# Optimization experiments

Hardware: AMD Instinct MI355X
Metric: run time of the kernel (lower is better)

Reference implementation:

```python
import jax, jax.numpy as jnp
import numpy as np

N = 16384      # number of points (pixels)
C = 64         # value channels of U
D_REF = 5      # bilateral reference feature dim (xy + rgb)


def setup_inputs() -> dict:
    key = jax.random.key(0)
    k1, k2 = jax.random.split(key)
    U = jax.random.normal(k1, (N, C), dtype=jnp.float32)
    ref = jax.random.normal(k2, (N, D_REF), dtype=jnp.float32)
    return {"U": U, "ref": ref}


def reference(U, ref):
    # Gaussian filtering on reference features (exact form of the LSH-approx filter):
    #   out[i] = sum_j exp(-0.5 * ||ref_i - ref_j||^2) * U[j]  -  U[i]
    sq = jnp.sum(ref * ref, axis=-1)                      # [N]
    d2 = sq[:, None] + sq[None, :] - 2.0 * (ref @ ref.T)  # [N, N] squared distances
    K = jnp.exp(-0.5 * jnp.maximum(d2, 0.0))              # [N, N] Gaussian kernel
    return K @ U - U                                       # [N, C]
```

## Files before the change

kernel.cpp:

```cpp
#include <hip/hip_runtime.h>
#include <hip/hip_bf16.h>
#include <stdint.h>

#define N_PTS 16384
#define C_CH  64
#define D_REF 5
#define LOG2E 1.44269504088896340736f
#define IBLOCKS 64

typedef __attribute__((ext_vector_type(8))) short bf16x8;
typedef __attribute__((ext_vector_type(4))) float f32x4;

__device__ __forceinline__ unsigned short bf16rn(float v) {
    unsigned u = __builtin_bit_cast(unsigned, v) + 0x8000u;
    return (unsigned short)(u >> 16);
}
__device__ __forceinline__ float bf16tof(unsigned x) {
    return __builtin_bit_cast(float, x << 16);
}
__device__ __forceinline__ unsigned pack2bf16(float lo, float hi) {
    unsigned a = __builtin_bit_cast(unsigned, lo) + 0x8000u;
    unsigned b = __builtin_bit_cast(unsigned, hi) + 0x8000u;
    return __builtin_amdgcn_perm(b, a, 0x07060302u);
}
__device__ __forceinline__ unsigned cvt2(float lo, float hi) {
#if __has_builtin(__builtin_amdgcn_cvt_pk_bf16_f32)
    typedef __attribute__((ext_vector_type(2))) __bf16 bf162_t;
    bf162_t r = __builtin_amdgcn_cvt_pk_bf16_f32(lo, hi);
    return __builtin_bit_cast(unsigned, r);
#else
    return pack2bf16(lo, hi);
#endif
}
__device__ __forceinline__ float fast_exp2(float x) {
#if __has_builtin(__builtin_amdgcn_exp2f)
    return __builtin_amdgcn_exp2f(x);
#else
    return exp2f(x);
#endif
}
__device__ __forceinline__ void dma16(const unsigned short* g, unsigned short* l) {
#if __has_builtin(__builtin_amdgcn_global_load_lds)
    __builtin_amdgcn_global_load_lds(
        (const __attribute__((address_space(1))) unsigned int*)g,
        (__attribute__((address_space(3))) unsigned int*)l, 16, 0, 0);
#else
    const int lane = threadIdx.x & 63;
    *(uint4*)(l + lane * 8) = *(const uint4*)(g);
#endif
}

__global__ __launch_bounds__(256) void prep_all(
    const float* __restrict__ U, const float* __restrict__ ref,
    unsigned short* __restrict__ packA, unsigned short* __restrict__ packB,
    unsigned short* __restrict__ utPack)
{
    __shared__ unsigned short tile[64 * 80];
    const int bid = blockIdx.x;
    const int t   = threadIdx.x;

    if (bid < 512) {
        const int gid  = bid * 256 + t;
        const int half = gid >> 16;
        const int id   = gid & 0xFFFF;
        const int tile16 = id >> 6;
        const int lane = id & 63;
        const int q    = lane >> 4;
        const int m    = lane & 15;
        const int p = half ? (tile16 * 16 + m)
                           : ((tile16 >> 1) * 32 + (m >> 2) * 8 + (m & 3) + (tile16 & 1) * 4);

        const float* r = ref + (size_t)p * D_REF;
        float rv[5];
        float sq = 0.f;
#pragma unroll
        for (int d = 0; d < 5; ++d) { rv[d] = r[d]; sq += rv[d] * rv[d]; }
        const float h = -0.5f * LOG2E * sq;

        unsigned short bh[5], bl[5];
#pragma unroll
        for (int d = 0; d < 5; ++d) {
            const float base = half ? rv[d] * LOG2E : rv[d];
            bh[d] = bf16rn(base);
            bl[d] = bf16rn(base - bf16tof((unsigned)bh[d]));
        }
        const unsigned short hh  = bf16rn(h);
        const unsigned short hl  = bf16rn(h - bf16tof((unsigned)hh));
        const unsigned short one = 0x3F80;

        unsigned short outv[8];
#pragma unroll
        for (int tt = 0; tt < 8; ++tt) {
            const int k = q * 8 + tt;
            unsigned short v = 0;
            if (!half) {
                if      (k < 5)   v = bh[k];
                else if (k < 10)  v = bh[k - 5];
                else if (k < 15)  v = bl[k - 10];
                else if (k == 15) v = hh;
                else if (k == 16) v = hl;
                else if (k <= 18) v = one;
            } else {
                if      (k < 5)   v = bh[k];
                else if (k < 10)  v = bl[k - 5];
                else if (k < 15)  v = bh[k - 10];
                else if (k <= 16) v = one;
                else if (k == 17) v = hh;
                else if (k == 18) v = hl;
            }
            outv[tt] = v;
        }
        unsigned short* dst = (half ? packB : packA) + ((size_t)tile16 * 64 + lane) * 8;
        *(uint4*)dst = *(uint4*)outv;
    } else {
        const int b  = bid - 512;
        const int j0 = b * 64;
        const int c  = t & 63;
        const int jb = t >> 6;
#pragma unroll
        for (int k = 0; k < 16; ++k) {
            const int jr = jb + k * 4;
            tile[c * 80 + jr] = bf16rn(U[(size_t)(j0 + jr) * C_CH + c]);
        }
        __syncthreads();
#pragma unroll
        for (int rep = 0; rep < 2; ++rep) {
            const int id   = rep * 256 + t;
            const int lane = id & 63;
            const int ct   = (id >> 6) & 3;
            const int kt   = id >> 8;
            const int m    = lane & 15;
            const int q    = lane >> 4;
            const uint4 frag = *(const uint4*)&tile[(ct * 16 + m) * 80 + kt * 32 + q * 8];
            const int jtile  = b * 2 + kt;
            *(uint4*)&utPack[(((size_t)jtile * 4 + ct) * 64 + lane) * 8] = frag;
        }
    }
}

template<int JS>
__global__ __launch_bounds__(256, 4) void lsh_main(
    const float* __restrict__ U,
    const unsigned short* __restrict__ packA,
    const unsigned short* __restrict__ packB,
    const unsigned short* __restrict__ utPack,
    unsigned short* __restrict__ part,
    float* __restrict__ out,
    int use_part)
{
    constexpr int UNITS  = (N_PTS / JS) / 32;
    constexpr int CUNITS = 4;
    constexpr int NCH    = UNITS / CUNITS;
    __shared__ __align__(16) unsigned short sh[2 * CUNITS * 2048];

    const int t    = threadIdx.x;
    const int lane = t & 63;
    const int wave = t >> 6;
    const int q    = lane >> 4;
    const int m    = lane & 15;

    const int ib = blockIdx.x / JS;
    const int js = blockIdx.x % JS;

    bf16x8 bfrag[4];
#pragma unroll
    for (int s = 0; s < 4; ++s) {
        const int itile = ib * 16 + wave * 4 + s;
        bfrag[s] = *(const bf16x8*)(packB + ((size_t)itile * 64 + lane) * 8);
    }

    f32x4 acc[4][4];
#pragma unroll
    for (int s = 0; s < 4; ++s)
#pragma unroll
        for (int ct = 0; ct < 4; ++ct) acc[s][ct] = (f32x4){0.f, 0.f, 0.f, 0.f};

    const unsigned short* pA = packA + ((size_t)js * UNITS) * 1024 + lane * 8;
    bf16x8 ga0 = *(const bf16x8*)pA;
    bf16x8 ga1 = *(const bf16x8*)(pA + 512);

    const unsigned short* srcU0 = utPack + ((size_t)js * UNITS) * 2048;
#pragma unroll
    for (int r = 0; r < CUNITS; ++r)
        dma16(srcU0 + (r * 4 + wave) * 512 + lane * 8, sh + (r * 4 + wave) * 512);
    __syncthreads();

    for (int ch = 0; ch < NCH; ++ch) {
        unsigned short* buf = sh + (ch & 1) * (CUNITS * 2048);
        if (ch + 1 < NCH) {
            const unsigned short* srcN = srcU0 + (size_t)(ch + 1) * (CUNITS * 2048);
            unsigned short* nbuf = sh + ((ch + 1) & 1) * (CUNITS * 2048);
#pragma unroll
            for (int r = 0; r < CUNITS; ++r)
                dma16(srcN + (r * 4 + wave) * 512 + lane * 8, nbuf + (r * 4 + wave) * 512);
        }

#pragma unroll
        for (int u4 = 0; u4 < CUNITS; ++u4) {
            const bf16x8 nga0 = *(const bf16x8*)(pA + 1024);
            const bf16x8 nga1 = *(const bf16x8*)(pA + 1536);

            const f32x4 z = (f32x4){0.f, 0.f, 0.f, 0.f};
            bf16x8 sfrag[4];
#pragma unroll
            for (int sp = 0; sp < 2; ++sp) {
                f32x4 g0a = __builtin_amdgcn_mfma_f32_16x16x32_bf16(ga0, bfrag[sp*2+0], z, 0, 0, 0);
                f32x4 g1a = __builtin_amdgcn_mfma_f32_16x16x32_bf16(ga1, bfrag[sp*2+0], z, 0, 0, 0);
                f32x4 g0b = __builtin_amdgcn_mfma_f32_16x16x32_bf16(ga0, bfrag[sp*2+1], z, 0, 0, 0);
                f32x4 g1b = __builtin_amdgcn_mfma_f32_16x16x32_bf16(ga1, bfrag[sp*2+1], z, 0, 0, 0);
                union { unsigned u[4]; bf16x8 v; } sa, sb;
                sa.u[0] = cvt2(fast_exp2(g0a[0]), fast_exp2(g0a[1]));
                sa.u[1] = cvt2(fast_exp2(g0a[2]), fast_exp2(g0a[3]));
                sa.u[2] = cvt2(fast_exp2(g1a[0]), fast_exp2(g1a[1]));
                sa.u[3] = cvt2(fast_exp2(g1a[2]), fast_exp2(g1a[3]));
                sb.u[0] = cvt2(fast_exp2(g0b[0]), fast_exp2(g0b[1]));
                sb.u[1] = cvt2(fast_exp2(g0b[2]), fast_exp2(g0b[3]));
                sb.u[2] = cvt2(fast_exp2(g1b[0]), fast_exp2(g1b[1]));
                sb.u[3] = cvt2(fast_exp2(g1b[2]), fast_exp2(g1b[3]));
                sfrag[sp*2+0] = sa.v;
                sfrag[sp*2+1] = sb.v;
            }
#pragma unroll
            for (int ct = 0; ct < 4; ++ct) {
                const bf16x8 uf = *(const bf16x8*)(buf + u4 * 2048 + ct * 512 + lane * 8);
#pragma unroll
                for (int s = 0; s < 4; ++s)
                    acc[s][ct] = __builtin_amdgcn_mfma_f32_16x16x32_bf16(
                        uf, sfrag[s], acc[s][ct], 0, 0, 0);
            }
            pA += 1024;
            ga0 = nga0;
            ga1 = nga1;
        }
        __syncthreads();
    }

    if (use_part) {
        unsigned short* dst = part + ((size_t)js * IBLOCKS + ib) * 16384;
#pragma unroll
        for (int s = 0; s < 4; ++s)
#pragma unroll
            for (int cp = 0; cp < 2; ++cp) {
                uint4 w;
                w.x = cvt2(acc[s][cp*2+0][0], acc[s][cp*2+0][1]);
                w.y = cvt2(acc[s][cp*2+0][2], acc[s][cp*2+0][3]);
                w.z = cvt2(acc[s][cp*2+1][0], acc[s][cp*2+1][1]);
                w.w = cvt2(acc[s][cp*2+1][2], acc[s][cp*2+1][3]);
                *(uint4*)(dst + ((s * 2 + cp) * 256 + t) * 8) = w;
            }
    } else {
#pragma unroll
        for (int s = 0; s < 4; ++s) {
            const int i_glob = ib * 256 + (wave * 4 + s) * 16 + m;
#pragma unroll
            for (int ct = 0; ct < 4; ++ct)
#pragma unroll
                for (int r2 = 0; r2 < 4; ++r2) {
                    const int c = ct * 16 + q * 4 + r2;
                    float val = acc[s][ct][r2];
                    if (js == 0) val -= U[(size_t)i_glob * C_CH + c];
                    atomicAdd(&out[(size_t)i_glob * C_CH + c], val);
                }
        }
    }
}

template<int JS>
__global__ __launch_bounds__(256) void reduce_part(
    const unsigned short* __restrict__ part, const f32x4* __restrict__ Uv,
    f32x4* __restrict__ out)
{
    const int x  = blockIdx.x * 256 + threadIdx.x;
    const int i  = x >> 4;
    const int c4 = (x & 15) * 4;
    const int blk = i >> 8, il = i & 255;
    const int wv = il >> 6, s = (il >> 4) & 3, mm = il & 15;
    const int ct = c4 >> 4, qq = (c4 >> 2) & 3;
    const int cp = ct >> 1, cti = ct & 1;
    const size_t off = (size_t)blk * 16384 +
        (size_t)(((s * 2 + cp) * 256) + (wv * 64 + qq * 16 + mm)) * 8 + cti * 4;
    float s0 = 0.f, s1 = 0.f, s2 = 0.f, s3 = 0.f;
#pragma unroll
    for (int js = 0; js < JS; ++js) {
        const uint2 w = *(const uint2*)(part + (size_t)js * (IBLOCKS * 16384) + off);
        s0 += bf16tof(w.x & 0xFFFFu);
        s1 += bf16tof(w.x >> 16);
        s2 += bf16tof(w.y & 0xFFFFu);
        s3 += bf16tof(w.y >> 16);
    }
    const f32x4 u = Uv[x];
    out[x] = (f32x4){s0 - u[0], s1 - u[1], s2 - u[2], s3 - u[3]};
}

extern "C" void kernel_launch(void* const* d_in, const int* in_sizes, int n_in,
                              void* d_out, int out_size, void* d_ws, size_t ws_size,
                              hipStream_t stream) {
    const float* U   = (const float*)d_in[0];
    const float* ref = (const float*)d_in[1];
    float* out = (float*)d_out;

    unsigned short* utPack = (unsigned short*)d_ws;
    unsigned short* packA  = (unsigned short*)((char*)d_ws + (size_t)2 * 1024 * 1024);
    unsigned short* packB  = (unsigned short*)((char*)d_ws + (size_t)3 * 1024 * 1024);
    unsigned short* part   = (unsigned short*)((char*)d_ws + (size_t)4 * 1024 * 1024);

    const size_t MB = 1024 * 1024;
    prep_all<<<768, 256, 0, stream>>>(U, ref, packA, packB, utPack);

    if (ws_size >= 36 * MB) {
        lsh_main<16><<<IBLOCKS * 16, 256, 0, stream>>>(U, packA, packB, utPack,
                                                       part, out, 1);
        reduce_part<16><<<1024, 256, 0, stream>>>(part, (const f32x4*)U, (f32x4*)out);
    } else {
        hipMemsetAsync(d_out, 0, (size_t)out_size * sizeof(float), stream);
        lsh_main<8><<<IBLOCKS * 8, 256, 0, stream>>>(U, packA, packB, utPack,
                                                     part, out, 0);
    }
}
```

Measured before the change: 137.1 us.

## Stage packA fragments through LDS with single-buffered chunk loads

Removes the double-buffered U pipeline and the per-wave global register prefetch of packA fragments. Each 128-column chunk now loads both the U tile and the A fragments into LDS with async DMA, synchronizes, then computes. The LDS footprint drops from 16K to 12K shorts, and each A fragment is fetched from global once per block instead of once per wave. In exchange, load latency is no longer overlapped with compute, and each chunk adds an extra barrier.

```diff
diff --git a/kernel.cpp b/kernel.cpp
--- a/kernel.cpp
+++ b/kernel.cpp
@@ -148,10 +148,8 @@
     float* __restrict__ out,
     int use_part)
 {
-    constexpr int UNITS  = (N_PTS / JS) / 32;
-    constexpr int CUNITS = 4;
-    constexpr int NCH    = UNITS / CUNITS;
-    __shared__ __align__(16) unsigned short sh[2 * CUNITS * 2048];
+    constexpr int CHUNKS = (N_PTS / JS) / 128;
+    __shared__ __align__(16) unsigned short sh[12288];
 
     const int t    = threadIdx.x;
     const int lane = t & 63;
@@ -175,64 +173,45 @@
 #pragma unroll
         for (int ct = 0; ct < 4; ++ct) acc[s][ct] = (f32x4){0.f, 0.f, 0.f, 0.f};
 
-    const unsigned short* pA = packA + ((size_t)js * UNITS) * 1024 + lane * 8;
-    bf16x8 ga0 = *(const bf16x8*)pA;
-    bf16x8 ga1 = *(const bf16x8*)(pA + 512);
-
-    const unsigned short* srcU0 = utPack + ((size_t)js * UNITS) * 2048;
-#pragma unroll
-    for (int r = 0; r < CUNITS; ++r)
-        dma16(srcU0 + (r * 4 + wave) * 512 + lane * 8, sh + (r * 4 + wave) * 512);
-    __syncthreads();
-
-    for (int ch = 0; ch < NCH; ++ch) {
-        unsigned short* buf = sh + (ch & 1) * (CUNITS * 2048);
-        if (ch + 1 < NCH) {
-            const unsigned short* srcN = srcU0 + (size_t)(ch + 1) * (CUNITS * 2048);
-            unsigned short* nbuf = sh + ((ch + 1) & 1) * (CUNITS * 2048);
-#pragma unroll
-            for (int r = 0; r < CUNITS; ++r)
-                dma16(srcN + (r * 4 + wave) * 512 + lane * 8, nbuf + (r * 4 + wave) * 512);
-        }
-
-#pragma unroll
-        for (int u4 = 0; u4 < CUNITS; ++u4) {
-            const bf16x8 nga0 = *(const bf16x8*)(pA + 1024);
-            const bf16x8 nga1 = *(const bf16x8*)(pA + 1536);
+    for (int chunk = 0; chunk < CHUNKS; ++chunk) {
+        const unsigned short* srcU = utPack + (size_t)(js * CHUNKS + chunk) * 8192;
+        const unsigned short* srcA = packA  + (size_t)(js * CHUNKS + chunk) * 4096;
+        __syncthreads();
+#pragma unroll
+        for (int r = 0; r < 4; ++r)
+            dma16(srcU + r * 2048 + wave * 512 + lane * 8, sh + r * 2048 + wave * 512);
+#pragma unroll
+        for (int r = 0; r < 2; ++r)
+            dma16(srcA + r * 2048 + wave * 512 + lane * 8, sh + 8192 + r * 2048 + wave * 512);
+        __syncthreads();
+
+#pragma unroll
+        for (int kt = 0; kt < 4; ++kt) {
+            const bf16x8 ga0 = *(const bf16x8*)(sh + 8192 + (kt * 2 + 0) * 512 + lane * 8);
+            const bf16x8 ga1 = *(const bf16x8*)(sh + 8192 + (kt * 2 + 1) * 512 + lane * 8);
 
             const f32x4 z = (f32x4){0.f, 0.f, 0.f, 0.f};
             bf16x8 sfrag[4];
 #pragma unroll
-            for (int sp = 0; sp < 2; ++sp) {
-                f32x4 g0a = __builtin_amdgcn_mfma_f32_16x16x32_bf16(ga0, bfrag[sp*2+0], z, 0, 0, 0);
-                f32x4 g1a = __builtin_amdgcn_mfma_f32_16x16x32_bf16(ga1, bfrag[sp*2+0], z, 0, 0, 0);
-                f32x4 g0b = __builtin_amdgcn_mfma_f32_16x16x32_bf16(ga0, bfrag[sp*2+1], z, 0, 0, 0);
-                f32x4 g1b = __builtin_amdgcn_mfma_f32_16x16x32_bf16(ga1, bfrag[sp*2+1], z, 0, 0, 0);
-                union { unsigned u[4]; bf16x8 v; } sa, sb;
-                sa.u[0] = cvt2(fast_exp2(g0a[0]), fast_exp2(g0a[1]));
-                sa.u[1] = cvt2(fast_exp2(g0a[2]), fast_exp2(g0a[3]));
-                sa.u[2] = cvt2(fast_exp2(g1a[0]), fast_exp2(g1a[1]));
-                sa.u[3] = cvt2(fast_exp2(g1a[2]), fast_exp2(g1a[3]));
-                sb.u[0] = cvt2(fast_exp2(g0b[0]), fast_exp2(g0b[1]));
-                sb.u[1] = cvt2(fast_exp2(g0b[2]), fast_exp2(g0b[3]));
-                sb.u[2] = cvt2(fast_exp2(g1b[0]), fast_exp2(g1b[1]));
-                sb.u[3] = cvt2(fast_exp2(g1b[2]), fast_exp2(g1b[3]));
-                sfrag[sp*2+0] = sa.v;
-                sfrag[sp*2+1] = sb.v;
+            for (int s = 0; s < 4; ++s) {
+                const f32x4 g0 = __builtin_amdgcn_mfma_f32_16x16x32_bf16(ga0, bfrag[s], z, 0, 0, 0);
+                const f32x4 g1 = __builtin_amdgcn_mfma_f32_16x16x32_bf16(ga1, bfrag[s], z, 0, 0, 0);
+                union { unsigned u[4]; bf16x8 v; } sb;
+                sb.u[0] = cvt2(fast_exp2(g0[0]), fast_exp2(g0[1]));
+                sb.u[1] = cvt2(fast_exp2(g0[2]), fast_exp2(g0[3]));
+                sb.u[2] = cvt2(fast_exp2(g1[0]), fast_exp2(g1[1]));
+                sb.u[3] = cvt2(fast_exp2(g1[2]), fast_exp2(g1[3]));
+                sfrag[s] = sb.v;
             }
 #pragma unroll
             for (int ct = 0; ct < 4; ++ct) {
-                const bf16x8 uf = *(const bf16x8*)(buf + u4 * 2048 + ct * 512 + lane * 8);
+                const bf16x8 uf = *(const bf16x8*)(sh + kt * 2048 + ct * 512 + lane * 8);
 #pragma unroll
                 for (int s = 0; s < 4; ++s)
                     acc[s][ct] = __builtin_amdgcn_mfma_f32_16x16x32_bf16(
                         uf, sfrag[s], acc[s][ct], 0, 0, 0);
             }
-            pA += 1024;
-            ga0 = nga0;
-            ga1 = nga1;
-        }
-        __syncthreads();
+        }
     }
 
     if (use_part) {
```

Result: faster. 122.8 us (-10.4%).
